# Optimization experiments

Hardware: AMD Instinct MI355X
Metric: run time of the kernel (lower is better)

The kernel has to match this reference:

```python
import jax, jax.numpy as jnp
import numpy as np

D_MODEL = 1024
N_HEADS = 16
HEAD_DIM = D_MODEL // N_HEADS
WINDOW = 256


def setup_inputs() -> dict:
    key = jax.random.key(0)
    k1, k2, k3 = jax.random.split(key, 3)
    B, T = 4, 2048
    x = jax.random.normal(k1, (B, T, D_MODEL), dtype=jnp.float32)
    # weights stored as [in, out] (torch Linear does x @ W.T with W [out,in])
    scale_qkv = 1.0 / np.sqrt(D_MODEL)
    w_qkv = jax.random.normal(k2, (D_MODEL, 3 * D_MODEL), dtype=jnp.float32) * scale_qkv
    w_out = jax.random.normal(k3, (D_MODEL, D_MODEL), dtype=jnp.float32) * scale_qkv
    return {"x": x, "w_qkv": w_qkv, "w_out": w_out}


def _sliding_window_attention(x, w_qkv, w_out):
    B, T, C = x.shape
    qkv = x @ w_qkv                              # [B,T,3C]
    q, k, v = jnp.split(qkv, 3, axis=-1)

    def reshape(t):
        return t.reshape(B, T, N_HEADS, HEAD_DIM).transpose(0, 2, 1, 3)  # [B,H,T,Dh]

    q, k, v = reshape(q), reshape(k), reshape(v)

    # banded causal mask: position i attends to j in [i-WINDOW, i]
    pos = jnp.arange(T)
    dist = pos[None, :] - pos[:, None]           # dist[i,j] = j - i
    blocked = (dist > 0) | (dist < -WINDOW)      # True = blocked

    scale = 1.0 / np.sqrt(HEAD_DIM)
    scores = jnp.einsum('bhqd,bhkd->bhqk', q, k) * scale
    scores = jnp.where(blocked[None, None], -jnp.inf, scores)
    attn = jax.nn.softmax(scores, axis=-1)
    out = jnp.einsum('bhqk,bhkd->bhqd', attn, v)
    out = out.transpose(0, 2, 1, 3).reshape(B, T, C)
    return out @ w_out


def reference(x, w_qkv, w_out):
    return _sliding_window_attention(x, w_qkv, w_out)
```

## Files before the change

kernel.cpp:

```cpp
#include <hip/hip_runtime.h>
#include <stdint.h>

#define D_MODEL 1024
#define NHEADS  16
#define WINDOW  256
#define BATCH   4
#define SEQ     2048
#define NROWS   (BATCH*SEQ)

using short8 = __attribute__((ext_vector_type(8))) short;
using f32x4  = __attribute__((ext_vector_type(4))) float;
using u32x4  = __attribute__((ext_vector_type(4))) uint32_t;
using u16x4  = __attribute__((ext_vector_type(4))) unsigned short;
typedef unsigned short u16;

__device__ __forceinline__ u16 f2b(float f) {
  union { float f; uint32_t u; } v; v.f = f;
  uint32_t r = v.u + 0x7fffu + ((v.u >> 16) & 1u);
  return (u16)(r >> 16);
}

__device__ __forceinline__ void gload_lds16(const void* g, void* l) {
  __builtin_amdgcn_global_load_lds(
      (const __attribute__((address_space(1))) uint32_t*)g,
      (__attribute__((address_space(3))) uint32_t*)l, 16, 0, 0);
}

__global__ void cvt_cast_kernel(const float* __restrict__ in, u16* __restrict__ out, int n4) {
  int i = blockIdx.x * blockDim.x + threadIdx.x;
  if (i < n4) {
    f32x4 v = *(const f32x4*)(in + 4 * (size_t)i);
    u16x4 o;
    o.x = f2b(v.x); o.y = f2b(v.y); o.z = f2b(v.z); o.w = f2b(v.w);
    *(u16x4*)(out + 4 * (size_t)i) = o;
  }
}

__global__ __launch_bounds__(256) void cvtT_kernel(const float* __restrict__ in, u16* __restrict__ out,
                                                   int K, int C) {
  __shared__ float T[64 * 65];
  const int nbn = C >> 6;
  const int bn = blockIdx.x % nbn, bk = blockIdx.x / nbn;
  const int tid = threadIdx.x;
#pragma unroll
  for (int it = 0; it < 4; ++it) {
    int c = it * 256 + tid;
    int k = c >> 4, g = c & 15;
    f32x4 v = *(const f32x4*)&in[(size_t)(bk * 64 + k) * C + bn * 64 + g * 4];
#pragma unroll
    for (int j = 0; j < 4; ++j) T[k * 65 + g * 4 + j] = v[j];
  }
  __syncthreads();
#pragma unroll
  for (int it = 0; it < 4; ++it) {
    int c = it * 256 + tid;
    int n = c >> 4, kg = c & 15;
    u16x4 o;
#pragma unroll
    for (int j = 0; j < 4; ++j) o[j] = f2b(T[(kg * 4 + j) * 65 + n]);
    *(u16x4*)&out[(size_t)(bn * 64 + n) * K + bk * 64 + kg * 4] = o;
  }
}

template <int MODE>
__global__ __launch_bounds__(512, 2) void gemm256_kernel(
    const u16* __restrict__ A, const u16* __restrict__ BT,
    u16* __restrict__ qk, u16* __restrict__ vT, float* __restrict__ outf,
    int M, int N, int K, int nbx) {
  __shared__ short SM[3 * 24576];

  const int tid = threadIdx.x;
  const int l = tid & 63;
  const int w = tid >> 6;
  const int wm = w >> 1, wn = w & 1;
  const int lr = l & 15, q = l >> 4;
  const int gsw = lr & 7;

  const int nwg = gridDim.x;
  const int lid = blockIdx.x;
  const int wg = (lid & 7) * (nwg >> 3) + (lid >> 3);
  const int bx = wg % nbx, by = wg / nbx;
  const int m0 = by * 256, n0 = bx * 128;

  const int NT = K >> 6;

  f32x4 acc[4][4] = {};

  auto stageA = [&](int slot, int kt) {
    short* As = SM + slot * 24576;
#pragma unroll
    for (int i = 0; i < 4; ++i) {
      int c = i * 512 + tid;
      int row = c >> 3;
      int gs = (c & 7) ^ (row & 7);
      gload_lds16(A + (size_t)(m0 + row) * K + (kt << 6) + gs * 8,
                  &As[(i * 512 + w * 64) * 8]);
    }
  };
  auto stageB = [&](int slot, int kt) {
    short* Bs = SM + slot * 24576 + 16384;
#pragma unroll
    for (int i = 0; i < 2; ++i) {
      int c = i * 512 + tid;
      int row = c >> 3;
      int gs = (c & 7) ^ (row & 7);
      gload_lds16(BT + (size_t)(n0 + row) * K + (kt << 6) + gs * 8,
                  &Bs[(i * 512 + w * 64) * 8]);
    }
  };

  stageA(0, 0); stageB(0, 0);
  stageA(1, 1); stageB(1, 1);

  int slot = 0;
  for (int t = 0; t < NT; ++t) {
    if (t + 1 < NT) { asm volatile("s_waitcnt vmcnt(6)" ::: "memory"); }
    else            { asm volatile("s_waitcnt vmcnt(0)" ::: "memory"); }
    __builtin_amdgcn_s_barrier();

    const short* As = SM + slot * 24576;
    const short* Bs = As + 16384;
    int s2 = slot + 2; if (s2 >= 3) s2 -= 3;
    const bool st = (t + 2 < NT);

#pragma unroll
    for (int kh = 0; kh < 2; ++kh) {
      short8 af[4], bfr[4];
      const int ko = (((kh << 2) | q) ^ gsw) * 8;
#pragma unroll
      for (int mf = 0; mf < 4; ++mf)
        af[mf] = *(const short8*)&As[(wm * 64 + mf * 16 + lr) * 64 + ko];
#pragma unroll
      for (int nf = 0; nf < 4; ++nf)
        bfr[nf] = *(const short8*)&Bs[(wn * 64 + nf * 16 + lr) * 64 + ko];
      if (st) { if (kh == 0) stageA(s2, t + 2); else stageB(s2, t + 2); }
      __builtin_amdgcn_s_barrier();
      asm volatile("s_waitcnt lgkmcnt(0)" ::: "memory");
      __builtin_amdgcn_s_setprio(1);
#pragma unroll
      for (int mf = 0; mf < 4; ++mf)
#pragma unroll
        for (int nf = 0; nf < 4; ++nf)
          acc[mf][nf] = __builtin_amdgcn_mfma_f32_16x16x32_bf16(af[mf], bfr[nf], acc[mf][nf], 0, 0, 0);
      __builtin_amdgcn_s_setprio(0);
    }
    slot = (slot + 1 == 3) ? 0 : slot + 1;
  }

  if (MODE == 1) {
#pragma unroll
    for (int mf = 0; mf < 4; ++mf) {
      const int m = m0 + wm * 64 + mf * 16 + q * 4;
#pragma unroll
      for (int nf = 0; nf < 4; ++nf) {
        const int n = n0 + wn * 64 + nf * 16 + lr;
#pragma unroll
        for (int r = 0; r < 4; ++r)
          outf[(size_t)(m + r) * N + n] = acc[mf][nf][r];
      }
    }
    return;
  }

  if (n0 < 2048) {
#pragma unroll
    for (int mf = 0; mf < 4; ++mf) {
      const int m = m0 + wm * 64 + mf * 16 + q * 4;
#pragma unroll
      for (int nf = 0; nf < 4; ++nf) {
        const int n = n0 + wn * 64 + nf * 16 + lr;
#pragma unroll
        for (int r = 0; r < 4; ++r)
          qk[(size_t)(m + r) * 2048 + n] = f2b(acc[mf][nf][r]);
      }
    }
  } else {
    __syncthreads();
    short* Tw = SM + w * 1152;
    const int b = by >> 3;
    const int head = (n0 - 2048 + wn * 64) >> 6;
    const int t0 = (by & 7) * 256 + wm * 64;
    const size_t dbase = ((size_t)(b * NHEADS + head)) * 64;
#pragma unroll
    for (int nf = 0; nf < 4; ++nf) {
#pragma unroll
      for (int mf = 0; mf < 4; ++mf)
#pragma unroll
        for (int r = 0; r < 4; ++r)
          Tw[lr * 72 + mf * 16 + q * 4 + r] = (short)f2b(acc[mf][nf][r]);
      asm volatile("s_waitcnt lgkmcnt(0)" ::: "memory");
#pragma unroll
      for (int it = 0; it < 2; ++it) {
        int c = it * 64 + l;
        int row = c >> 3, off = (c & 7) * 8;
        short8 v = *(const short8*)&Tw[row * 72 + off];
        *(short8*)&vT[(dbase + nf * 16 + row) * 2048 + t0 + off] = v;
      }
      asm volatile("s_waitcnt lgkmcnt(0)" ::: "memory");
    }
  }
}

__global__ __launch_bounds__(256) void attn_kernel(
    const u16* __restrict__ qk, const u16* __restrict__ vT, u16* __restrict__ attn) {
  __shared__ short Ks[2][64 * 72];
  __shared__ short Vs[2][64 * 72];
  __shared__ short Ps[4 * 16 * 72];

  const int tid = threadIdx.x;
  const int l = tid & 63;
  const int w = tid >> 6;

  const int lid = blockIdx.x;
  const int xcd = lid & 7, slot = lid >> 3;
  const int bh = (slot >> 5) * 8 + xcd;
  const int qt = slot & 31;
  const int b = bh >> 4, h = bh & 15;
  const int qbase = qt * 64;
  const size_t rowbase = (size_t)b * 2048;
  const int lr = l & 15, lk = (l >> 4) * 8;

  const int row0 = tid >> 3,          off0 = (tid & 7) * 8;
  const int row1 = (256 + tid) >> 3,  off1 = ((256 + tid) & 7) * 8;

  u32x4 kreg0, kreg1, vreg0, vreg1;
  auto load_regs = [&](int kt) {
    const int kbase = kt * 64;
    kreg0 = *(const u32x4*)&qk[(rowbase + kbase + row0) * 2048 + 1024 + h * 64 + off0];
    kreg1 = *(const u32x4*)&qk[(rowbase + kbase + row1) * 2048 + 1024 + h * 64 + off1];
    vreg0 = *(const u32x4*)&vT[((size_t)bh * 64 + row0) * 2048 + kbase + off0];
    vreg1 = *(const u32x4*)&vT[((size_t)bh * 64 + row1) * 2048 + kbase + off1];
  };
  auto write_lds = [&](int buf) {
    *(u32x4*)&Ks[buf][row0 * 72 + off0] = kreg0;
    *(u32x4*)&Ks[buf][row1 * 72 + off1] = kreg1;
    *(u32x4*)&Vs[buf][row0 * 72 + off0] = vreg0;
    *(u32x4*)&Vs[buf][row1 * 72 + off1] = vreg1;
  };

  const size_t qrowg = (rowbase + qbase + w * 16 + lr) * 2048 + h * 64;
  short8 aq0 = *(const short8*)&qk[qrowg + lk];
  short8 aq1 = *(const short8*)&qk[qrowg + 32 + lk];

  float lsum[4] = {0.f, 0.f, 0.f, 0.f};
  f32x4 o[4] = {};

  int kt0 = qt - 4; if (kt0 < 0) kt0 = 0;

  load_regs(kt0);
  write_lds(0);
  if (kt0 + 1 <= qt) load_regs(kt0 + 1);
  asm volatile("s_waitcnt lgkmcnt(0)" ::: "memory");
  __builtin_amdgcn_s_barrier();

  int cur = 0;
  for (int kt = kt0; kt <= qt; ++kt) {
    const int kbase = kt * 64;

    f32x4 s[4] = {};
    __builtin_amdgcn_s_setprio(1);
#pragma unroll
    for (int fn = 0; fn < 4; ++fn) {
      short8 bk0 = *(const short8*)&Ks[cur][(fn * 16 + lr) * 72 + lk];
      short8 bk1 = *(const short8*)&Ks[cur][(fn * 16 + lr) * 72 + 32 + lk];
      s[fn] = __builtin_amdgcn_mfma_f32_16x16x32_bf16(aq0, bk0, s[fn], 0, 0, 0);
      s[fn] = __builtin_amdgcn_mfma_f32_16x16x32_bf16(aq1, bk1, s[fn], 0, 0, 0);
    }
    __builtin_amdgcn_s_setprio(0);

    f32x4 p[4];
    if (kt == qt || kt == qt - 4) {
      const int qrow0 = qbase + w * 16 + (l >> 4) * 4;
#pragma unroll
      for (int fn = 0; fn < 4; ++fn) {
        int kj = kbase + fn * 16 + lr;
#pragma unroll
        for (int r = 0; r < 4; ++r) {
          int qi = qrow0 + r;
          bool ok = (kj <= qi) && (kj >= qi - WINDOW);
          p[fn][r] = ok ? __expf(s[fn][r] * 0.125f) : 0.f;
        }
      }
    } else {
#pragma unroll
      for (int fn = 0; fn < 4; ++fn)
#pragma unroll
        for (int r = 0; r < 4; ++r)
          p[fn][r] = __expf(s[fn][r] * 0.125f);
    }
#pragma unroll
    for (int r = 0; r < 4; ++r)
      lsum[r] += (p[0][r] + p[1][r]) + (p[2][r] + p[3][r]);

    short* Pw = &Ps[w * 16 * 72];
#pragma unroll
    for (int fn = 0; fn < 4; ++fn)
#pragma unroll
      for (int r = 0; r < 4; ++r)
        Pw[((l >> 4) * 4 + r) * 72 + fn * 16 + lr] = (short)f2b(p[fn][r]);
    asm volatile("s_waitcnt lgkmcnt(0)" ::: "memory");

    __builtin_amdgcn_s_setprio(1);
#pragma unroll
    for (int ks = 0; ks < 2; ++ks) {
      short8 pa = *(const short8*)&Pw[lr * 72 + ks * 32 + lk];
#pragma unroll
      for (int fd = 0; fd < 4; ++fd) {
        short8 vb = *(const short8*)&Vs[cur][(fd * 16 + lr) * 72 + ks * 32 + lk];
        o[fd] = __builtin_amdgcn_mfma_f32_16x16x32_bf16(pa, vb, o[fd], 0, 0, 0);
      }
    }
    __builtin_amdgcn_s_setprio(0);
    asm volatile("s_waitcnt lgkmcnt(0)" ::: "memory");

    if (kt + 1 <= qt) {
      write_lds(cur ^ 1);
      if (kt + 2 <= qt) load_regs(kt + 2);
      asm volatile("s_waitcnt lgkmcnt(0)" ::: "memory");
      __builtin_amdgcn_s_barrier();
      cur ^= 1;
    }
  }

#pragma unroll
  for (int off = 1; off < 16; off <<= 1)
#pragma unroll
    for (int r = 0; r < 4; ++r) lsum[r] += __shfl_xor(lsum[r], off);

#pragma unroll
  for (int fd = 0; fd < 4; ++fd) {
#pragma unroll
    for (int r = 0; r < 4; ++r) {
      int m = qbase + w * 16 + (l >> 4) * 4 + r;
      float val = o[fd][r] / lsum[r];
      attn[(rowbase + m) * 1024 + h * 64 + fd * 16 + lr] = f2b(val);
    }
  }
}

extern "C" void kernel_launch(void* const* d_in, const int* in_sizes, int n_in,
                              void* d_out, int out_size, void* d_ws, size_t ws_size,
                              hipStream_t stream) {
  const float* x     = (const float*)d_in[0];
  const float* w_qkv = (const float*)d_in[1];
  const float* w_out = (const float*)d_in[2];
  float* out = (float*)d_out;
  uint8_t* ws = (uint8_t*)d_ws;

  u16* xb    = (u16*)(ws + 0);
  u16* wqkvT = (u16*)(ws + 16777216);
  u16* woutT = (u16*)(ws + 23068672);
  u16* qk    = (u16*)(ws + 25165824);
  u16* vT    = (u16*)(ws + 58720256);

  cvt_cast_kernel<<<(NROWS * D_MODEL / 4 + 255) / 256, 256, 0, stream>>>(x, xb, NROWS * D_MODEL / 4);
  cvtT_kernel<<<(3 * D_MODEL / 64) * (D_MODEL / 64), 256, 0, stream>>>(w_qkv, wqkvT, D_MODEL, 3 * D_MODEL);
  cvtT_kernel<<<(D_MODEL / 64) * (D_MODEL / 64), 256, 0, stream>>>(w_out, woutT, D_MODEL, D_MODEL);

  gemm256_kernel<0><<<(3 * D_MODEL / 128) * (NROWS / 256), 512, 0, stream>>>(
      xb, wqkvT, qk, vT, nullptr, NROWS, 3 * D_MODEL, D_MODEL, 3 * D_MODEL / 128);

  attn_kernel<<<BATCH * NHEADS * (SEQ / 64), 256, 0, stream>>>(qk, vT, xb);

  gemm256_kernel<1><<<(D_MODEL / 128) * (NROWS / 256), 512, 0, stream>>>(
      xb, woutT, nullptr, nullptr, out, NROWS, D_MODEL, D_MODEL, D_MODEL / 128);
}
```

Before: 128.2 us.

## Share K/V tiles across two query tiles per attention block; fuse conversion kernels

The attention kernel now uses 512 threads per block, covering two adjacent 64-row query tiles that share one set of K/V tile loads across a union window of six key tiles. Each four-wave group skips the key tiles outside its own band. The three fp32-to-bf16 conversion kernels are merged into one launch. This is meant to reduce redundant K/V global loads and launch overhead, at the cost of idle waves on non-overlapping tiles and half as many attention blocks.

```diff
diff --git a/kernel.cpp b/kernel.cpp
--- a/kernel.cpp
+++ b/kernel.cpp
@@ -26,22 +26,8 @@
       (__attribute__((address_space(3))) uint32_t*)l, 16, 0, 0);
 }
 
-__global__ void cvt_cast_kernel(const float* __restrict__ in, u16* __restrict__ out, int n4) {
-  int i = blockIdx.x * blockDim.x + threadIdx.x;
-  if (i < n4) {
-    f32x4 v = *(const f32x4*)(in + 4 * (size_t)i);
-    u16x4 o;
-    o.x = f2b(v.x); o.y = f2b(v.y); o.z = f2b(v.z); o.w = f2b(v.w);
-    *(u16x4*)(out + 4 * (size_t)i) = o;
-  }
-}
-
-__global__ __launch_bounds__(256) void cvtT_kernel(const float* __restrict__ in, u16* __restrict__ out,
-                                                   int K, int C) {
-  __shared__ float T[64 * 65];
-  const int nbn = C >> 6;
-  const int bn = blockIdx.x % nbn, bk = blockIdx.x / nbn;
-  const int tid = threadIdx.x;
+__device__ __forceinline__ void cvtT_body(const float* __restrict__ in, u16* __restrict__ out,
+                                          int K, int C, int bn, int bk, int tid, float* T) {
 #pragma unroll
   for (int it = 0; it < 4; ++it) {
     int c = it * 256 + tid;
@@ -59,6 +45,27 @@
 #pragma unroll
     for (int j = 0; j < 4; ++j) o[j] = f2b(T[(kg * 4 + j) * 65 + n]);
     *(u16x4*)&out[(size_t)(bn * 64 + n) * K + bk * 64 + kg * 4] = o;
+  }
+}
+
+__global__ __launch_bounds__(256) void cvt_all_kernel(
+    const float* __restrict__ x, const float* __restrict__ w_qkv, const float* __restrict__ w_out,
+    u16* __restrict__ xb, u16* __restrict__ wqkvT, u16* __restrict__ woutT) {
+  __shared__ float T[64 * 65];
+  const int bid = blockIdx.x;
+  const int tid = threadIdx.x;
+  if (bid < 8192) {
+    int i = bid * 256 + tid;
+    f32x4 v = *(const f32x4*)(x + 4 * (size_t)i);
+    u16x4 o;
+    o.x = f2b(v.x); o.y = f2b(v.y); o.z = f2b(v.z); o.w = f2b(v.w);
+    *(u16x4*)(xb + 4 * (size_t)i) = o;
+  } else if (bid < 8192 + 768) {
+    int b2 = bid - 8192;
+    cvtT_body(w_qkv, wqkvT, D_MODEL, 3 * D_MODEL, b2 % 48, b2 / 48, tid, T);
+  } else {
+    int b3 = bid - 8960;
+    cvtT_body(w_out, woutT, D_MODEL, D_MODEL, b3 % 16, b3 / 16, tid, T);
   }
 }
 
@@ -201,121 +208,124 @@
   }
 }
 
-__global__ __launch_bounds__(256) void attn_kernel(
+__global__ __launch_bounds__(512) void attn_kernel(
     const u16* __restrict__ qk, const u16* __restrict__ vT, u16* __restrict__ attn) {
   __shared__ short Ks[2][64 * 72];
   __shared__ short Vs[2][64 * 72];
-  __shared__ short Ps[4 * 16 * 72];
+  __shared__ short Ps[8 * 16 * 72];
 
   const int tid = threadIdx.x;
   const int l = tid & 63;
   const int w = tid >> 6;
+  const int wset = w >> 2;
+  const int wl = w & 3;
 
   const int lid = blockIdx.x;
   const int xcd = lid & 7, slot = lid >> 3;
-  const int bh = (slot >> 5) * 8 + xcd;
-  const int qt = slot & 31;
+  const int bh = (slot >> 4) * 8 + xcd;
+  const int qt2 = slot & 15;
+  const int qtA = qt2 * 2;
+  const int myqt = qtA + wset;
+  const int qbase = myqt * 64;
   const int b = bh >> 4, h = bh & 15;
-  const int qbase = qt * 64;
   const size_t rowbase = (size_t)b * 2048;
   const int lr = l & 15, lk = (l >> 4) * 8;
 
-  const int row0 = tid >> 3,          off0 = (tid & 7) * 8;
-  const int row1 = (256 + tid) >> 3,  off1 = ((256 + tid) & 7) * 8;
-
-  u32x4 kreg0, kreg1, vreg0, vreg1;
+  const int srow = tid >> 3, soff = (tid & 7) * 8;
+
+  u32x4 kreg, vreg;
   auto load_regs = [&](int kt) {
     const int kbase = kt * 64;
-    kreg0 = *(const u32x4*)&qk[(rowbase + kbase + row0) * 2048 + 1024 + h * 64 + off0];
-    kreg1 = *(const u32x4*)&qk[(rowbase + kbase + row1) * 2048 + 1024 + h * 64 + off1];
-    vreg0 = *(const u32x4*)&vT[((size_t)bh * 64 + row0) * 2048 + kbase + off0];
-    vreg1 = *(const u32x4*)&vT[((size_t)bh * 64 + row1) * 2048 + kbase + off1];
+    kreg = *(const u32x4*)&qk[(rowbase + kbase + srow) * 2048 + 1024 + h * 64 + soff];
+    vreg = *(const u32x4*)&vT[((size_t)bh * 64 + srow) * 2048 + kbase + soff];
   };
   auto write_lds = [&](int buf) {
-    *(u32x4*)&Ks[buf][row0 * 72 + off0] = kreg0;
-    *(u32x4*)&Ks[buf][row1 * 72 + off1] = kreg1;
-    *(u32x4*)&Vs[buf][row0 * 72 + off0] = vreg0;
-    *(u32x4*)&Vs[buf][row1 * 72 + off1] = vreg1;
+    *(u32x4*)&Ks[buf][srow * 72 + soff] = kreg;
+    *(u32x4*)&Vs[buf][srow * 72 + soff] = vreg;
   };
 
-  const size_t qrowg = (rowbase + qbase + w * 16 + lr) * 2048 + h * 64;
+  const size_t qrowg = (rowbase + qbase + wl * 16 + lr) * 2048 + h * 64;
   short8 aq0 = *(const short8*)&qk[qrowg + lk];
   short8 aq1 = *(const short8*)&qk[qrowg + 32 + lk];
 
   float lsum[4] = {0.f, 0.f, 0.f, 0.f};
   f32x4 o[4] = {};
 
-  int kt0 = qt - 4; if (kt0 < 0) kt0 = 0;
-
-  load_regs(kt0);
+  int ktlo = qtA - 4; if (ktlo < 0) ktlo = 0;
+  const int kthi = qtA + 1;
+
+  load_regs(ktlo);
   write_lds(0);
-  if (kt0 + 1 <= qt) load_regs(kt0 + 1);
+  load_regs(ktlo + 1);
   asm volatile("s_waitcnt lgkmcnt(0)" ::: "memory");
   __builtin_amdgcn_s_barrier();
 
+  short* Pw = &Ps[w * 16 * 72];
   int cur = 0;
-  for (int kt = kt0; kt <= qt; ++kt) {
+  for (int kt = ktlo; kt <= kthi; ++kt) {
     const int kbase = kt * 64;
-
-    f32x4 s[4] = {};
-    __builtin_amdgcn_s_setprio(1);
-#pragma unroll
-    for (int fn = 0; fn < 4; ++fn) {
-      short8 bk0 = *(const short8*)&Ks[cur][(fn * 16 + lr) * 72 + lk];
-      short8 bk1 = *(const short8*)&Ks[cur][(fn * 16 + lr) * 72 + 32 + lk];
-      s[fn] = __builtin_amdgcn_mfma_f32_16x16x32_bf16(aq0, bk0, s[fn], 0, 0, 0);
-      s[fn] = __builtin_amdgcn_mfma_f32_16x16x32_bf16(aq1, bk1, s[fn], 0, 0, 0);
-    }
-    __builtin_amdgcn_s_setprio(0);
-
-    f32x4 p[4];
-    if (kt == qt || kt == qt - 4) {
-      const int qrow0 = qbase + w * 16 + (l >> 4) * 4;
+    const bool active = wset ? (kt >= myqt - 4) : (kt <= myqt);
+
+    if (active) {
+      f32x4 s[4] = {};
+      __builtin_amdgcn_s_setprio(1);
 #pragma unroll
       for (int fn = 0; fn < 4; ++fn) {
-        int kj = kbase + fn * 16 + lr;
-#pragma unroll
-        for (int r = 0; r < 4; ++r) {
-          int qi = qrow0 + r;
-          bool ok = (kj <= qi) && (kj >= qi - WINDOW);
-          p[fn][r] = ok ? __expf(s[fn][r] * 0.125f) : 0.f;
+        short8 bk0 = *(const short8*)&Ks[cur][(fn * 16 + lr) * 72 + lk];
+        short8 bk1 = *(const short8*)&Ks[cur][(fn * 16 + lr) * 72 + 32 + lk];
+        s[fn] = __builtin_amdgcn_mfma_f32_16x16x32_bf16(aq0, bk0, s[fn], 0, 0, 0);
+        s[fn] = __builtin_amdgcn_mfma_f32_16x16x32_bf16(aq1, bk1, s[fn], 0, 0, 0);
+      }
+      __builtin_amdgcn_s_setprio(0);
+
+      f32x4 p[4];
+      if (kt == myqt || kt == myqt - 4) {
+        const int qrow0 = qbase + wl * 16 + (l >> 4) * 4;
+#pragma unroll
+        for (int fn = 0; fn < 4; ++fn) {
+          int kj = kbase + fn * 16 + lr;
+#pragma unroll
+          for (int r = 0; r < 4; ++r) {
+            int qi = qrow0 + r;
+            bool ok = (kj <= qi) && (kj >= qi - WINDOW);
+            p[fn][r] = ok ? __expf(s[fn][r] * 0.125f) : 0.f;
+          }
         }
-      }
-    } else {
+      } else {
+#pragma unroll
+        for (int fn = 0; fn < 4; ++fn)
+#pragma unroll
+          for (int r = 0; r < 4; ++r)
+            p[fn][r] = __expf(s[fn][r] * 0.125f);
+      }
+#pragma unroll
+      for (int r = 0; r < 4; ++r)
+        lsum[r] += (p[0][r] + p[1][r]) + (p[2][r] + p[3][r]);
+
 #pragma unroll
       for (int fn = 0; fn < 4; ++fn)
 #pragma unroll
         for (int r = 0; r < 4; ++r)
-          p[fn][r] = __expf(s[fn][r] * 0.125f);
-    }
-#pragma unroll
-    for (int r = 0; r < 4; ++r)
-      lsum[r] += (p[0][r] + p[1][r]) + (p[2][r] + p[3][r]);
-
-    short* Pw = &Ps[w * 16 * 72];
-#pragma unroll
-    for (int fn = 0; fn < 4; ++fn)
-#pragma unroll
-      for (int r = 0; r < 4; ++r)
-        Pw[((l >> 4) * 4 + r) * 72 + fn * 16 + lr] = (short)f2b(p[fn][r]);
-    asm volatile("s_waitcnt lgkmcnt(0)" ::: "memory");
-
-    __builtin_amdgcn_s_setprio(1);
-#pragma unroll
-    for (int ks = 0; ks < 2; ++ks) {
-      short8 pa = *(const short8*)&Pw[lr * 72 + ks * 32 + lk];
-#pragma unroll
-      for (int fd = 0; fd < 4; ++fd) {
-        short8 vb = *(const short8*)&Vs[cur][(fd * 16 + lr) * 72 + ks * 32 + lk];
-        o[fd] = __builtin_amdgcn_mfma_f32_16x16x32_bf16(pa, vb, o[fd], 0, 0, 0);
-      }
-    }
-    __builtin_amdgcn_s_setprio(0);
-    asm volatile("s_waitcnt lgkmcnt(0)" ::: "memory");
-
-    if (kt + 1 <= qt) {
+          Pw[((l >> 4) * 4 + r) * 72 + fn * 16 + lr] = (short)f2b(p[fn][r]);
+      asm volatile("s_waitcnt lgkmcnt(0)" ::: "memory");
+
+      __builtin_amdgcn_s_setprio(1);
+#pragma unroll
+      for (int ks = 0; ks < 2; ++ks) {
+        short8 pa = *(const short8*)&Pw[lr * 72 + ks * 32 + lk];
+#pragma unroll
+        for (int fd = 0; fd < 4; ++fd) {
+          short8 vb = *(const short8*)&Vs[cur][(fd * 16 + lr) * 72 + ks * 32 + lk];
+          o[fd] = __builtin_amdgcn_mfma_f32_16x16x32_bf16(pa, vb, o[fd], 0, 0, 0);
+        }
+      }
+      __builtin_amdgcn_s_setprio(0);
+      asm volatile("s_waitcnt lgkmcnt(0)" ::: "memory");
+    }
+
+    if (kt + 1 <= kthi) {
       write_lds(cur ^ 1);
-      if (kt + 2 <= qt) load_regs(kt + 2);
+      if (kt + 2 <= kthi) load_regs(kt + 2);
       asm volatile("s_waitcnt lgkmcnt(0)" ::: "memory");
       __builtin_amdgcn_s_barrier();
       cur ^= 1;
@@ -331,7 +341,7 @@
   for (int fd = 0; fd < 4; ++fd) {
 #pragma unroll
     for (int r = 0; r < 4; ++r) {
-      int m = qbase + w * 16 + (l >> 4) * 4 + r;
+      int m = qbase + wl * 16 + (l >> 4) * 4 + r;
       float val = o[fd][r] / lsum[r];
       attn[(rowbase + m) * 1024 + h * 64 + fd * 16 + lr] = f2b(val);
     }
@@ -353,14 +363,12 @@
   u16* qk    = (u16*)(ws + 25165824);
   u16* vT    = (u16*)(ws + 58720256);
 
-  cvt_cast_kernel<<<(NROWS * D_MODEL / 4 + 255) / 256, 256, 0, stream>>>(x, xb, NROWS * D_MODEL / 4);
-  cvtT_kernel<<<(3 * D_MODEL / 64) * (D_MODEL / 64), 256, 0, stream>>>(w_qkv, wqkvT, D_MODEL, 3 * D_MODEL);
-  cvtT_kernel<<<(D_MODEL / 64) * (D_MODEL / 64), 256, 0, stream>>>(w_out, woutT, D_MODEL, D_MODEL);
+  cvt_all_kernel<<<8192 + 768 + 256, 256, 0, stream>>>(x, w_qkv, w_out, xb, wqkvT, woutT);
 
   gemm256_kernel<0><<<(3 * D_MODEL / 128) * (NROWS / 256), 512, 0, stream>>>(
       xb, wqkvT, qk, vT, nullptr, NROWS, 3 * D_MODEL, D_MODEL, 3 * D_MODEL / 128);
 
-  attn_kernel<<<BATCH * NHEADS * (SEQ / 64), 256, 0, stream>>>(qk, vT, xb);
+  attn_kernel<<<BATCH * NHEADS * (SEQ / 128), 512, 0, stream>>>(qk, vT, xb);
 
   gemm256_kernel<1><<<(D_MODEL / 128) * (NROWS / 256), 512, 0, stream>>>(
       xb, woutT, nullptr, nullptr, out, NROWS, D_MODEL, D_MODEL, D_MODEL / 128);
```

Result: faster. 123.7 us (-3.5%).
